# Optimization experiments

Measured on AMD Instinct MI355X. Metric: run time of the kernel, lower is better.

The kernel has to match this reference:

```python
import jax, jax.numpy as jnp
import numpy as np

B, L, D_MODEL = 1, 1024, 768
H = 12            # num_heads == num_key_value_heads
FDIM = 16         # feature_dim
HEAD_DIM = D_MODEL // H  # 64
EPS = 1e-12
R2 = np.sqrt(2.0)
RD = np.sqrt(float(FDIM))        # sqrt(16) = 4
RRD = np.sqrt(RD)                # sqrt(4) = 2


def setup_inputs() -> dict:
    key = jax.random.key(0)
    ks = jax.random.split(key, 5)
    s = 1.0 / np.sqrt(D_MODEL)
    return {
        "hidden_states": jax.random.normal(ks[0], (B, L, D_MODEL), dtype=jnp.float32),
        "Wq": jax.random.normal(ks[1], (D_MODEL, H * FDIM), dtype=jnp.float32) * s,
        "Wk": jax.random.normal(ks[2], (D_MODEL, H * FDIM), dtype=jnp.float32) * s,
        "Wv": jax.random.normal(ks[3], (D_MODEL, D_MODEL), dtype=jnp.float32) * s,
        "Wo": jax.random.normal(ks[4], (D_MODEL, D_MODEL), dtype=jnp.float32) * s,
    }


def taylor_exp_feature_map(x):
    # x: (b, h, l, FDIM) -> (b, h, l, 1 + FDIM + FDIM^2)
    x2 = (x[..., :, None] * x[..., None, :]).reshape(*x.shape[:-1], FDIM * FDIM) / R2
    ones = jnp.ones((*x.shape[:-1], 1), dtype=x.dtype)
    return jnp.concatenate([ones, x / RRD, x2 / RD], axis=-1)


def reference(hidden_states, Wq, Wk, Wv, Wo):
    b, l, _ = hidden_states.shape
    q = (hidden_states @ Wq).reshape(b, l, H, FDIM).transpose(0, 2, 1, 3)
    k = (hidden_states @ Wk).reshape(b, l, H, FDIM).transpose(0, 2, 1, 3)
    v = (hidden_states @ Wv).reshape(b, l, H, HEAD_DIM).transpose(0, 2, 1, 3)
    q = taylor_exp_feature_map(q)  # (b,h,l,Dexp)
    k = taylor_exp_feature_map(k)  # (b,h,l,Dexp)
    # causal linear attention: y_t = q_t . cumsum_t(k_s v_s^T) / (q_t . cumsum_t(k_s) + eps)
    kv = k[..., :, None] * v[..., None, :]          # (b,h,l,Dexp,hd)
    kv_cum = jnp.cumsum(kv, axis=2)                  # (b,h,l,Dexp,hd)
    num = jnp.einsum('bhln,bhlnd->bhld', q, kv_cum)  # (b,h,l,hd)
    k_cum = jnp.cumsum(k, axis=2)                    # (b,h,l,Dexp)
    den = jnp.einsum('bhln,bhln->bhl', q, k_cum)[..., None] + EPS
    y = num / den                                    # (b,h,l,hd)
    y = y.transpose(0, 2, 1, 3).reshape(b, l, H * HEAD_DIM)
    return y @ Wo
```

## Files before the change

### kernel.cpp

```cpp
#include <hip/hip_runtime.h>

#define C2 0.17677669529663687f

typedef __attribute__((ext_vector_type(8))) short short8;
typedef __attribute__((ext_vector_type(8))) unsigned short ushort8;
typedef __attribute__((ext_vector_type(4))) float f32x4;

__device__ __forceinline__ unsigned short f2bf(float x) {
    union { float f; unsigned u; } v; v.f = x;
    unsigned r = v.u + 0x7fffu + ((v.u >> 16) & 1u);
    return (unsigned short)(r >> 16);
}
__device__ __forceinline__ float bf2f(unsigned short u) {
    union { unsigned u; float f; } v; v.u = ((unsigned)u) << 16;
    return v.f;
}

__device__ __forceinline__ void gemm_inblk_splitk(
    const float* __restrict__ A, const float* __restrict__ W,
    float* __restrict__ out, int row0, int n0, int outcol0, int ldw, int outld)
{
    __shared__ unsigned short Al[2][2][64][40];
    __shared__ unsigned short Bl[2][2][64][40];
    __shared__ float red[64][65];
    const int tid = threadIdx.x;
    const int g = tid >> 8;
    const int t = tid & 255;
    const int lane = t & 63, wave4 = t >> 6;
    const int wm = wave4 & 1, wn = wave4 >> 1;
    const int quad = lane >> 4, lr = lane & 15;
    const int k0base = g * 384;

    f32x4 acc[2][2] = {{{0.f,0.f,0.f,0.f},{0.f,0.f,0.f,0.f}},
                       {{0.f,0.f,0.f,0.f},{0.f,0.f,0.f,0.f}}};

    float4 ra[2], rb[2];
    #pragma unroll
    for (int l = 0; l < 2; ++l) {
        int idx = t + l * 256;
        ra[l] = *(const float4*)&A[(size_t)(row0 + (idx >> 3)) * 768 + k0base + (idx & 7) * 4];
        rb[l] = *(const float4*)&W[(size_t)(k0base + (idx >> 4)) * ldw + n0 + (idx & 15) * 4];
    }
    #pragma unroll
    for (int l = 0; l < 2; ++l) {
        int idx = t + l * 256;
        *(ushort4*)&Al[g][0][idx >> 3][(idx & 7) * 4] =
            make_ushort4(f2bf(ra[l].x), f2bf(ra[l].y), f2bf(ra[l].z), f2bf(ra[l].w));
        int kr = idx >> 4, nq = (idx & 15) * 4;
        int col = (((kr >> 3) ^ ((idx & 15) >> 2)) << 3) | (kr & 7);
        Bl[g][0][nq + 0][col] = f2bf(rb[l].x);
        Bl[g][0][nq + 1][col] = f2bf(rb[l].y);
        Bl[g][0][nq + 2][col] = f2bf(rb[l].z);
        Bl[g][0][nq + 3][col] = f2bf(rb[l].w);
    }
    __syncthreads();

    const int ITER = 12;
    #pragma unroll
    for (int i = 0; i < ITER; ++i) {
        const int cur = i & 1, nxt = cur ^ 1;
        float4 na[2], nb[2];
        if (i + 1 < ITER) {
            int kn = k0base + (i + 1) * 32;
            #pragma unroll
            for (int l = 0; l < 2; ++l) {
                int idx = t + l * 256;
                na[l] = *(const float4*)&A[(size_t)(row0 + (idx >> 3)) * 768 + kn + (idx & 7) * 4];
                nb[l] = *(const float4*)&W[(size_t)(kn + (idx >> 4)) * ldw + n0 + (idx & 15) * 4];
            }
        }
        short8 af[2], bfr[2];
        #pragma unroll
        for (int mi = 0; mi < 2; ++mi)
            af[mi] = *(const short8*)&Al[g][cur][wm * 32 + mi * 16 + lr][quad << 3];
        #pragma unroll
        for (int ni = 0; ni < 2; ++ni) {
            int csw = quad ^ ((wn * 2 + ni) & 3);
            bfr[ni] = *(const short8*)&Bl[g][cur][wn * 32 + ni * 16 + lr][csw << 3];
        }
        #pragma unroll
        for (int mi = 0; mi < 2; ++mi)
            #pragma unroll
            for (int ni = 0; ni < 2; ++ni)
                acc[mi][ni] = __builtin_amdgcn_mfma_f32_16x16x32_bf16(af[mi], bfr[ni], acc[mi][ni], 0, 0, 0);
        if (i + 1 < ITER) {
            #pragma unroll
            for (int l = 0; l < 2; ++l) {
                int idx = t + l * 256;
                *(ushort4*)&Al[g][nxt][idx >> 3][(idx & 7) * 4] =
                    make_ushort4(f2bf(na[l].x), f2bf(na[l].y), f2bf(na[l].z), f2bf(na[l].w));
                int kr = idx >> 4, nq = (idx & 15) * 4;
                int col = (((kr >> 3) ^ ((idx & 15) >> 2)) << 3) | (kr & 7);
                Bl[g][nxt][nq + 0][col] = f2bf(nb[l].x);
                Bl[g][nxt][nq + 1][col] = f2bf(nb[l].y);
                Bl[g][nxt][nq + 2][col] = f2bf(nb[l].z);
                Bl[g][nxt][nq + 3][col] = f2bf(nb[l].w);
            }
        }
        __syncthreads();
    }
    if (g == 1) {
        #pragma unroll
        for (int mi = 0; mi < 2; ++mi)
            #pragma unroll
            for (int ni = 0; ni < 2; ++ni)
                #pragma unroll
                for (int r = 0; r < 4; ++r)
                    red[wm * 32 + mi * 16 + quad * 4 + r][wn * 32 + ni * 16 + lr] = acc[mi][ni][r];
    }
    __syncthreads();
    if (g == 0) {
        #pragma unroll
        for (int mi = 0; mi < 2; ++mi)
            #pragma unroll
            for (int ni = 0; ni < 2; ++ni)
                #pragma unroll
                for (int r = 0; r < 4; ++r) {
                    int rr = wm * 32 + mi * 16 + quad * 4 + r;
                    int cc = wn * 32 + ni * 16 + lr;
                    out[(size_t)(row0 + rr) * outld + outcol0 + cc] = acc[mi][ni][r] + red[rr][cc];
                }
    }
}

__global__ __launch_bounds__(512) void gemm_qkv_mfma(
    const float* __restrict__ H, const float* __restrict__ Wq,
    const float* __restrict__ Wk, const float* __restrict__ Wv,
    float* __restrict__ out)
{
    const int nt = blockIdx.x, mt = blockIdx.y;
    const float* W; int ldw, n0;
    if (nt < 3)      { W = Wq; ldw = 192; n0 = nt * 64; }
    else if (nt < 6) { W = Wk; ldw = 192; n0 = (nt - 3) * 64; }
    else             { W = Wv; ldw = 768; n0 = (nt - 6) * 64; }
    gemm_inblk_splitk(H, W, out, mt * 64, n0, nt * 64, ldw, 1152);
}

__global__ __launch_bounds__(512) void gemm_wo_mfma(
    const float* __restrict__ Y, const float* __restrict__ Wo, float* __restrict__ out)
{
    const int nt = blockIdx.x, mt = blockIdx.y;
    gemm_inblk_splitk(Y, Wo, out, mt * 64, nt * 64, nt * 64, 768, 768);
}

__global__ __launch_bounds__(256) void chunk_state_k(
    const float* __restrict__ qkv, unsigned short* __restrict__ St, float* __restrict__ z)
{
    const int c = blockIdx.x, h = blockIdx.y;
    __shared__ float Kc[64][17];
    __shared__ unsigned short Pk[320][72];
    __shared__ unsigned short Vt[80][72];
    const int tid = threadIdx.x;
    const int lane = tid & 63, wave = tid >> 6;
    const int quad = lane >> 4, lr = lane & 15;

    {
        int s = tid >> 2, f4 = (tid & 3) * 4;
        float4 kv = *(const float4*)&qkv[(size_t)(c * 64 + s) * 1152 + 192 + h * 16 + f4];
        Kc[s][f4 + 0] = kv.x; Kc[s][f4 + 1] = kv.y; Kc[s][f4 + 2] = kv.z; Kc[s][f4 + 3] = kv.w;
    }
    #pragma unroll
    for (int l = 0; l < 4; ++l) {
        int idx = tid + l * 256;
        int s = idx >> 4, d4 = (idx & 15) * 4;
        float4 vv = *(const float4*)&qkv[(size_t)(c * 64 + s) * 1152 + 384 + h * 64 + d4];
        Vt[d4 + 0][s] = f2bf(vv.x);
        Vt[d4 + 1][s] = f2bf(vv.y);
        Vt[d4 + 2][s] = f2bf(vv.z);
        Vt[d4 + 3][s] = f2bf(vv.w);
    }
    for (int idx = tid; idx < 16 * 72; idx += 256) {
        int rr = 64 + idx / 72, ss = idx % 72;
        Vt[rr][ss] = (rr == 64 && ss < 64) ? (unsigned short)0x3F80 : (unsigned short)0;
    }
    __syncthreads();
    for (int idx = tid; idx < 2880; idx += 256) {
        int n = idx / 9, s8 = (idx % 9) * 8;
        short8 v8;
        #pragma unroll
        for (int tt = 0; tt < 8; ++tt) {
            int s = s8 + tt;
            float ph = 0.f;
            if (s < 64 && n < 273) {
                if (n == 0) ph = 1.f;
                else if (n < 17) ph = Kc[s][n - 1] * 0.5f;
                else { int m = n - 17; ph = Kc[s][m >> 4] * Kc[s][m & 15] * C2; }
            }
            v8[tt] = (short)f2bf(ph);
        }
        *(short8*)&Pk[n][s8] = v8;
    }
    __syncthreads();

    f32x4 acc[5][5];
    #pragma unroll
    for (int a = 0; a < 5; ++a)
        #pragma unroll
        for (int b = 0; b < 5; ++b) acc[a][b] = (f32x4){0.f, 0.f, 0.f, 0.f};
    #pragma unroll
    for (int ks = 0; ks < 2; ++ks) {
        short8 af[5], bfr[5];
        #pragma unroll
        for (int mt = 0; mt < 5; ++mt)
            af[mt] = *(const short8*)&Vt[mt * 16 + lr][ks * 32 + quad * 8];
        #pragma unroll
        for (int nt = 0; nt < 5; ++nt)
            bfr[nt] = *(const short8*)&Pk[(wave * 5 + nt) * 16 + lr][ks * 32 + quad * 8];
        #pragma unroll
        for (int mt = 0; mt < 5; ++mt)
            #pragma unroll
            for (int nt = 0; nt < 5; ++nt)
                acc[mt][nt] = __builtin_amdgcn_mfma_f32_16x16x32_bf16(af[mt], bfr[nt], acc[mt][nt], 0, 0, 0);
    }
    unsigned short* Sbt = St + (size_t)(h * 16 + c) * 18432;
    float* zb = z + (h * 16 + c) * 273;
    #pragma unroll
    for (int nt = 0; nt < 5; ++nt) {
        int n = (wave * 5 + nt) * 16 + lr;
        if (n < 288) {
            #pragma unroll
            for (int mt = 0; mt < 4; ++mt)
                #pragma unroll
                for (int r = 0; r < 4; ++r)
                    Sbt[(mt * 16 + quad * 4 + r) * 288 + n] =
                        (n < 273) ? f2bf(acc[mt][nt][r]) : (unsigned short)0;
            if (quad == 0 && n < 273) zb[n] = acc[4][nt][0];
        }
    }
}

__global__ __launch_bounds__(256) void scan_state_k(unsigned short* __restrict__ St, float* __restrict__ z)
{
    const int NV = 12 * 64 * 36;
    int gid = blockIdx.x * 256 + threadIdx.x;
    if (gid < NV) {
        int hh = gid / (64 * 36), rem = gid % (64 * 36);
        int d = rem / 36, nb = rem % 36;
        unsigned short* p = St + (size_t)hh * 16 * 18432 + d * 288 + nb * 8;
        ushort8 v[16];
        #pragma unroll
        for (int cc = 0; cc < 16; ++cc) v[cc] = *(const ushort8*)(p + (size_t)cc * 18432);
        float run[8] = {0.f,0.f,0.f,0.f,0.f,0.f,0.f,0.f};
        #pragma unroll
        for (int cc = 0; cc < 16; ++cc) {
            ushort8 w;
            #pragma unroll
            for (int j = 0; j < 8; ++j) {
                w[j] = f2bf(run[j]);
                run[j] += bf2f(v[cc][j]);
            }
            *(ushort8*)(p + (size_t)cc * 18432) = w;
        }
    } else if (gid < NV + 12 * 273) {
        int e2 = gid - NV, hh = e2 / 273, n = e2 % 273;
        float* p = z + hh * 16 * 273 + n;
        float v[16];
        #pragma unroll
        for (int cc = 0; cc < 16; ++cc) v[cc] = p[cc * 273];
        float run = 0.f;
        #pragma unroll
        for (int cc = 0; cc < 16; ++cc) { p[cc * 273] = run; run += v[cc]; }
    }
}

__global__ __launch_bounds__(256) void chunk_out_k(
    const float* __restrict__ qkv, const unsigned short* __restrict__ St, const float* __restrict__ z,
    float* __restrict__ y)
{
    const int c = blockIdx.x, h = blockIdx.y;
    __shared__ float Qc[64][17];
    __shared__ unsigned short Aq[64][40];
    __shared__ unsigned short Kb[64][40];
    __shared__ unsigned short Pq[64][360];
    __shared__ unsigned short Vt[64][72];
    __shared__ float zl[288];
    __shared__ float dpart[6][64];
    const int tid = threadIdx.x;
    const int lane = tid & 63, wave = tid >> 6;
    const int wm = wave & 1, wn = wave >> 1;
    const int quad = lane >> 4, lr = lane & 15;

    const unsigned short* Sgt = St + (size_t)(h * 16 + c) * 18432;
    short8 sfr[2][9];
    #pragma unroll
    for (int ni = 0; ni < 2; ++ni)
        #pragma unroll
        for (int ks = 0; ks < 9; ++ks)
            sfr[ni][ks] = *(const short8*)&Sgt[(wn * 32 + ni * 16 + lr) * 288 + ks * 32 + quad * 8];

    {
        int s = tid >> 2, f4 = (tid & 3) * 4;
        const float* base = &qkv[(size_t)(c * 64 + s) * 1152 + h * 16];
        float4 qv = *(const float4*)&base[f4];
        float4 kv = *(const float4*)&base[192 + f4];
        Qc[s][f4 + 0] = qv.x; Qc[s][f4 + 1] = qv.y; Qc[s][f4 + 2] = qv.z; Qc[s][f4 + 3] = qv.w;
        *(ushort4*)&Aq[s][f4] = make_ushort4(f2bf(qv.x), f2bf(qv.y), f2bf(qv.z), f2bf(qv.w));
        *(ushort4*)&Kb[s][f4] = make_ushort4(f2bf(kv.x), f2bf(kv.y), f2bf(kv.z), f2bf(kv.w));
        *(ushort4*)&Aq[s][16 + (tid & 3) * 4] = make_ushort4(0, 0, 0, 0);
        *(ushort4*)&Kb[s][16 + (tid & 3) * 4] = make_ushort4(0, 0, 0, 0);
    }
    #pragma unroll
    for (int l = 0; l < 4; ++l) {
        int idx = tid + l * 256;
        int ss = idx >> 4, d4 = (idx & 15) * 4;
        float4 vv = *(const float4*)&qkv[(size_t)(c * 64 + ss) * 1152 + 384 + h * 64 + d4];
        Vt[d4 + 0][ss] = f2bf(vv.x);
        Vt[d4 + 1][ss] = f2bf(vv.y);
        Vt[d4 + 2][ss] = f2bf(vv.z);
        Vt[d4 + 3][ss] = f2bf(vv.w);
    }
    const float* zg = z + (h * 16 + c) * 273;
    for (int idx = tid; idx < 288; idx += 256) zl[idx] = (idx < 273) ? zg[idx] : 0.f;
    __syncthreads();

    f32x4 accS[2][2] = {{{0.f,0.f,0.f,0.f},{0.f,0.f,0.f,0.f}},
                        {{0.f,0.f,0.f,0.f},{0.f,0.f,0.f,0.f}}};
    {
        short8 af[2], bfr[2];
        #pragma unroll
        for (int mi = 0; mi < 2; ++mi)
            af[mi] = *(const short8*)&Aq[wm * 32 + mi * 16 + lr][quad * 8];
        #pragma unroll
        for (int ni = 0; ni < 2; ++ni)
            bfr[ni] = *(const short8*)&Kb[wn * 32 + ni * 16 + lr][quad * 8];
        #pragma unroll
        for (int mi = 0; mi < 2; ++mi)
            #pragma unroll
            for (int ni = 0; ni < 2; ++ni)
                accS[mi][ni] = __builtin_amdgcn_mfma_f32_16x16x32_bf16(af[mi], bfr[ni], accS[mi][ni], 0, 0, 0);
    }

    {
        int i = lane;
        float qr[16];
        #pragma unroll
        for (int f = 0; f < 16; ++f) qr[f] = Qc[i][f];
        float dp = 0.f;
        int n0 = wave * 72;
        for (int n = n0; n < n0 + 72; ++n) {
            float ph;
            if (n == 0) ph = 1.f;
            else if (n < 17) ph = qr[n - 1] * 0.5f;
            else if (n < 273) { int m = n - 17; ph = qr[m >> 4] * qr[m & 15] * C2; }
            else ph = 0.f;
            Pq[i][n] = f2bf(ph);
            dp += ph * zl[n];
        }
        dpart[wave][i] = dp;
    }

    #pragma unroll
    for (int mi = 0; mi < 2; ++mi) {
        float rs[4] = {0.f, 0.f, 0.f, 0.f};
        #pragma unroll
        for (int ni = 0; ni < 2; ++ni)
            #pragma unroll
            for (int r = 0; r < 4; ++r) {
                int i = wm * 32 + mi * 16 + quad * 4 + r;
                int j = wn * 32 + ni * 16 + lr;
                float u = accS[mi][ni][r];
                float sc = (j <= i) ? (1.f + 0.25f * u + u * u * (1.f / 32.f)) : 0.f;
                rs[r] += sc;
                Pq[i][288 + j] = f2bf(sc);
            }
        #pragma unroll
        for (int r = 0; r < 4; ++r) {
            float v = rs[r];
            v += __shfl_xor(v, 1);
            v += __shfl_xor(v, 2);
            v += __shfl_xor(v, 4);
            v += __shfl_xor(v, 8);
            if (lr == 0) dpart[4 + wn][wm * 32 + mi * 16 + quad * 4 + r] = v;
        }
    }
    __syncthreads();

    f32x4 acc[2][2] = {{{0.f,0.f,0.f,0.f},{0.f,0.f,0.f,0.f}},
                       {{0.f,0.f,0.f,0.f},{0.f,0.f,0.f,0.f}}};
    #pragma unroll
    for (int ks = 0; ks < 11; ++ks) {
        short8 af[2], bfr[2];
        #pragma unroll
        for (int mi = 0; mi < 2; ++mi)
            af[mi] = *(const short8*)&Pq[wm * 32 + mi * 16 + lr][ks * 32 + quad * 8];
        #pragma unroll
        for (int ni = 0; ni < 2; ++ni)
            bfr[ni] = (ks < 9)
                ? sfr[ni][ks]
                : *(const short8*)&Vt[wn * 32 + ni * 16 + lr][(ks - 9) * 32 + quad * 8];
        #pragma unroll
        for (int mi = 0; mi < 2; ++mi)
            #pragma unroll
            for (int ni = 0; ni < 2; ++ni)
                acc[mi][ni] = __builtin_amdgcn_mfma_f32_16x16x32_bf16(af[mi], bfr[ni], acc[mi][ni], 0, 0, 0);
    }

    #pragma unroll
    for (int mi = 0; mi < 2; ++mi)
        #pragma unroll
        for (int r = 0; r < 4; ++r) {
            int i = wm * 32 + mi * 16 + quad * 4 + r;
            float den = dpart[0][i] + dpart[1][i] + dpart[2][i] +
                        dpart[3][i] + dpart[4][i] + dpart[5][i] + 1e-12f;
            float rden = 1.f / den;
            #pragma unroll
            for (int ni = 0; ni < 2; ++ni)
                y[(size_t)(c * 64 + i) * 768 + h * 64 + wn * 32 + ni * 16 + lr] = acc[mi][ni][r] * rden;
        }
}

extern "C" void kernel_launch(void* const* d_in, const int* in_sizes, int n_in,
                              void* d_out, int out_size, void* d_ws, size_t ws_size,
                              hipStream_t stream) {
    const float* hs = (const float*)d_in[0];
    const float* Wq = (const float*)d_in[1];
    const float* Wk = (const float*)d_in[2];
    const float* Wv = (const float*)d_in[3];
    const float* Wo = (const float*)d_in[4];
    float* out = (float*)d_out;
    float* ws  = (float*)d_ws;

    float* qkv = ws;
    float* yb  = ws + 1179648;
    unsigned short* St = (unsigned short*)(ws + 1966080);
    float* zb  = ws + 5320704;

    gemm_qkv_mfma<<<dim3(18, 16), 512, 0, stream>>>(hs, Wq, Wk, Wv, qkv);
    chunk_state_k<<<dim3(16, 12), 256, 0, stream>>>(qkv, St, zb);
    scan_state_k <<<121, 256, 0, stream>>>(St, zb);
    chunk_out_k  <<<dim3(16, 12), 256, 0, stream>>>(qkv, St, zb, yb);
    gemm_wo_mfma <<<dim3(12, 16), 512, 0, stream>>>(yb, Wo, out);
}
```

Measured before the change: 134.9 us.

## Double waves per block in chunk state and output kernels

Both chunk kernels move from 256 to 512 threads (8 waves), and the MFMA tile work is split across more waves. chunk_state_k now assigns the 20 N-tiles round-robin across waves, and chunk_out_k gives each wave a 16-column slice with 12 denominator partials. With only 192 blocks, the intent is more in-flight waves per block to hide latency and spread MFMA and feature-map work. This costs extra reduction partials, some idle waves in the round-robin split, and fewer registers per thread.

```diff
diff --git a/kernel.cpp b/kernel.cpp
--- a/kernel.cpp
+++ b/kernel.cpp
@@ -143,8 +143,8 @@
     gemm_inblk_splitk(Y, Wo, out, mt * 64, nt * 64, nt * 64, 768, 768);
 }
 
-__global__ __launch_bounds__(256) void chunk_state_k(
-    const float* __restrict__ qkv, unsigned short* __restrict__ St, float* __restrict__ z)
+__global__ __launch_bounds__(512) void chunk_state_k(
+    const float* __restrict__ qkv, unsigned short* __restrict__ St, float* __restrict__ zb)
 {
     const int c = blockIdx.x, h = blockIdx.y;
     __shared__ float Kc[64][17];
@@ -154,14 +154,14 @@
     const int lane = tid & 63, wave = tid >> 6;
     const int quad = lane >> 4, lr = lane & 15;
 
-    {
+    if (tid < 256) {
         int s = tid >> 2, f4 = (tid & 3) * 4;
         float4 kv = *(const float4*)&qkv[(size_t)(c * 64 + s) * 1152 + 192 + h * 16 + f4];
         Kc[s][f4 + 0] = kv.x; Kc[s][f4 + 1] = kv.y; Kc[s][f4 + 2] = kv.z; Kc[s][f4 + 3] = kv.w;
     }
     #pragma unroll
-    for (int l = 0; l < 4; ++l) {
-        int idx = tid + l * 256;
+    for (int l = 0; l < 2; ++l) {
+        int idx = tid + l * 512;
         int s = idx >> 4, d4 = (idx & 15) * 4;
         float4 vv = *(const float4*)&qkv[(size_t)(c * 64 + s) * 1152 + 384 + h * 64 + d4];
         Vt[d4 + 0][s] = f2bf(vv.x);
@@ -169,12 +169,12 @@
         Vt[d4 + 2][s] = f2bf(vv.z);
         Vt[d4 + 3][s] = f2bf(vv.w);
     }
-    for (int idx = tid; idx < 16 * 72; idx += 256) {
+    for (int idx = tid; idx < 16 * 72; idx += 512) {
         int rr = 64 + idx / 72, ss = idx % 72;
         Vt[rr][ss] = (rr == 64 && ss < 64) ? (unsigned short)0x3F80 : (unsigned short)0;
     }
     __syncthreads();
-    for (int idx = tid; idx < 2880; idx += 256) {
+    for (int idx = tid; idx < 2880; idx += 512) {
         int n = idx / 9, s8 = (idx % 9) * 8;
         short8 v8;
         #pragma unroll
@@ -192,39 +192,44 @@
     }
     __syncthreads();
 
-    f32x4 acc[5][5];
-    #pragma unroll
-    for (int a = 0; a < 5; ++a)
-        #pragma unroll
-        for (int b = 0; b < 5; ++b) acc[a][b] = (f32x4){0.f, 0.f, 0.f, 0.f};
+    f32x4 acc[5][3];
+    #pragma unroll
+    for (int mt = 0; mt < 5; ++mt)
+        #pragma unroll
+        for (int nt = 0; nt < 3; ++nt) acc[mt][nt] = (f32x4){0.f, 0.f, 0.f, 0.f};
     #pragma unroll
     for (int ks = 0; ks < 2; ++ks) {
-        short8 af[5], bfr[5];
+        short8 af[5], bfr[3];
         #pragma unroll
         for (int mt = 0; mt < 5; ++mt)
             af[mt] = *(const short8*)&Vt[mt * 16 + lr][ks * 32 + quad * 8];
         #pragma unroll
-        for (int nt = 0; nt < 5; ++nt)
-            bfr[nt] = *(const short8*)&Pk[(wave * 5 + nt) * 16 + lr][ks * 32 + quad * 8];
+        for (int nt = 0; nt < 3; ++nt)
+            if (wave + 8 * nt < 20)
+                bfr[nt] = *(const short8*)&Pk[(wave + 8 * nt) * 16 + lr][ks * 32 + quad * 8];
         #pragma unroll
         for (int mt = 0; mt < 5; ++mt)
             #pragma unroll
-            for (int nt = 0; nt < 5; ++nt)
-                acc[mt][nt] = __builtin_amdgcn_mfma_f32_16x16x32_bf16(af[mt], bfr[nt], acc[mt][nt], 0, 0, 0);
+            for (int nt = 0; nt < 3; ++nt)
+                if (wave + 8 * nt < 20)
+                    acc[mt][nt] = __builtin_amdgcn_mfma_f32_16x16x32_bf16(af[mt], bfr[nt], acc[mt][nt], 0, 0, 0);
     }
     unsigned short* Sbt = St + (size_t)(h * 16 + c) * 18432;
-    float* zb = z + (h * 16 + c) * 273;
-    #pragma unroll
-    for (int nt = 0; nt < 5; ++nt) {
-        int n = (wave * 5 + nt) * 16 + lr;
-        if (n < 288) {
-            #pragma unroll
-            for (int mt = 0; mt < 4; ++mt)
+    float* zp = zb + (h * 16 + c) * 273;
+    #pragma unroll
+    for (int nt = 0; nt < 3; ++nt) {
+        int tile = wave + 8 * nt;
+        if (tile < 20) {
+            int n = tile * 16 + lr;
+            if (n < 288) {
                 #pragma unroll
-                for (int r = 0; r < 4; ++r)
-                    Sbt[(mt * 16 + quad * 4 + r) * 288 + n] =
-                        (n < 273) ? f2bf(acc[mt][nt][r]) : (unsigned short)0;
-            if (quad == 0 && n < 273) zb[n] = acc[4][nt][0];
+                for (int mt = 0; mt < 4; ++mt)
+                    #pragma unroll
+                    for (int r = 0; r < 4; ++r)
+                        Sbt[(mt * 16 + quad * 4 + r) * 288 + n] =
+                            (n < 273) ? f2bf(acc[mt][nt][r]) : (unsigned short)0;
+                if (quad == 0 && n < 273) zp[n] = acc[4][nt][0];
+            }
         }
     }
 }
@@ -263,7 +268,7 @@
     }
 }
 
-__global__ __launch_bounds__(256) void chunk_out_k(
+__global__ __launch_bounds__(512) void chunk_out_k(
     const float* __restrict__ qkv, const unsigned short* __restrict__ St, const float* __restrict__ z,
     float* __restrict__ y)
 {
@@ -274,21 +279,19 @@
     __shared__ unsigned short Pq[64][360];
     __shared__ unsigned short Vt[64][72];
     __shared__ float zl[288];
-    __shared__ float dpart[6][64];
+    __shared__ float dpart[12][64];
     const int tid = threadIdx.x;
     const int lane = tid & 63, wave = tid >> 6;
+    const int quad = lane >> 4, lr = lane & 15;
     const int wm = wave & 1, wn = wave >> 1;
-    const int quad = lane >> 4, lr = lane & 15;
 
     const unsigned short* Sgt = St + (size_t)(h * 16 + c) * 18432;
-    short8 sfr[2][9];
-    #pragma unroll
-    for (int ni = 0; ni < 2; ++ni)
-        #pragma unroll
-        for (int ks = 0; ks < 9; ++ks)
-            sfr[ni][ks] = *(const short8*)&Sgt[(wn * 32 + ni * 16 + lr) * 288 + ks * 32 + quad * 8];
-
-    {
+    short8 sfr[9];
+    #pragma unroll
+    for (int ks = 0; ks < 9; ++ks)
+        sfr[ks] = *(const short8*)&Sgt[(wn * 16 + lr) * 288 + ks * 32 + quad * 8];
+
+    if (tid < 256) {
         int s = tid >> 2, f4 = (tid & 3) * 4;
         const float* base = &qkv[(size_t)(c * 64 + s) * 1152 + h * 16];
         float4 qv = *(const float4*)&base[f4];
@@ -300,8 +303,8 @@
         *(ushort4*)&Kb[s][16 + (tid & 3) * 4] = make_ushort4(0, 0, 0, 0);
     }
     #pragma unroll
-    for (int l = 0; l < 4; ++l) {
-        int idx = tid + l * 256;
+    for (int l = 0; l < 2; ++l) {
+        int idx = tid + l * 512;
         int ss = idx >> 4, d4 = (idx & 15) * 4;
         float4 vv = *(const float4*)&qkv[(size_t)(c * 64 + ss) * 1152 + 384 + h * 64 + d4];
         Vt[d4 + 0][ss] = f2bf(vv.x);
@@ -310,24 +313,17 @@
         Vt[d4 + 3][ss] = f2bf(vv.w);
     }
     const float* zg = z + (h * 16 + c) * 273;
-    for (int idx = tid; idx < 288; idx += 256) zl[idx] = (idx < 273) ? zg[idx] : 0.f;
-    __syncthreads();
-
-    f32x4 accS[2][2] = {{{0.f,0.f,0.f,0.f},{0.f,0.f,0.f,0.f}},
-                        {{0.f,0.f,0.f,0.f},{0.f,0.f,0.f,0.f}}};
+    for (int idx = tid; idx < 288; idx += 512) zl[idx] = (idx < 273) ? zg[idx] : 0.f;
+    __syncthreads();
+
+    f32x4 accS[2] = {{0.f,0.f,0.f,0.f},{0.f,0.f,0.f,0.f}};
     {
-        short8 af[2], bfr[2];
-        #pragma unroll
-        for (int mi = 0; mi < 2; ++mi)
-            af[mi] = *(const short8*)&Aq[wm * 32 + mi * 16 + lr][quad * 8];
-        #pragma unroll
-        for (int ni = 0; ni < 2; ++ni)
-            bfr[ni] = *(const short8*)&Kb[wn * 32 + ni * 16 + lr][quad * 8];
-        #pragma unroll
-        for (int mi = 0; mi < 2; ++mi)
-            #pragma unroll
-            for (int ni = 0; ni < 2; ++ni)
-                accS[mi][ni] = __builtin_amdgcn_mfma_f32_16x16x32_bf16(af[mi], bfr[ni], accS[mi][ni], 0, 0, 0);
+        short8 bfr = *(const short8*)&Kb[wn * 16 + lr][quad * 8];
+        #pragma unroll
+        for (int mi = 0; mi < 2; ++mi) {
+            short8 af = *(const short8*)&Aq[wm * 32 + mi * 16 + lr][quad * 8];
+            accS[mi] = __builtin_amdgcn_mfma_f32_16x16x32_bf16(af, bfr, accS[mi], 0, 0, 0);
+        }
     }
 
     {
@@ -336,8 +332,8 @@
         #pragma unroll
         for (int f = 0; f < 16; ++f) qr[f] = Qc[i][f];
         float dp = 0.f;
-        int n0 = wave * 72;
-        for (int n = n0; n < n0 + 72; ++n) {
+        int n0 = wave * 36;
+        for (int n = n0; n < n0 + 36; ++n) {
             float ph;
             if (n == 0) ph = 1.f;
             else if (n < 17) ph = qr[n - 1] * 0.5f;
@@ -351,18 +347,16 @@
 
     #pragma unroll
     for (int mi = 0; mi < 2; ++mi) {
-        float rs[4] = {0.f, 0.f, 0.f, 0.f};
-        #pragma unroll
-        for (int ni = 0; ni < 2; ++ni)
-            #pragma unroll
-            for (int r = 0; r < 4; ++r) {
-                int i = wm * 32 + mi * 16 + quad * 4 + r;
-                int j = wn * 32 + ni * 16 + lr;
-                float u = accS[mi][ni][r];
-                float sc = (j <= i) ? (1.f + 0.25f * u + u * u * (1.f / 32.f)) : 0.f;
-                rs[r] += sc;
-                Pq[i][288 + j] = f2bf(sc);
-            }
+        float rs[4];
+        #pragma unroll
+        for (int r = 0; r < 4; ++r) {
+            int i = wm * 32 + mi * 16 + quad * 4 + r;
+            int j = wn * 16 + lr;
+            float u = accS[mi][r];
+            float sc = (j <= i) ? (1.f + 0.25f * u + u * u * (1.f / 32.f)) : 0.f;
+            rs[r] = sc;
+            Pq[i][288 + j] = f2bf(sc);
+        }
         #pragma unroll
         for (int r = 0; r < 4; ++r) {
             float v = rs[r];
@@ -370,29 +364,22 @@
             v += __shfl_xor(v, 2);
             v += __shfl_xor(v, 4);
             v += __shfl_xor(v, 8);
-            if (lr == 0) dpart[4 + wn][wm * 32 + mi * 16 + quad * 4 + r] = v;
-        }
-    }
-    __syncthreads();
-
-    f32x4 acc[2][2] = {{{0.f,0.f,0.f,0.f},{0.f,0.f,0.f,0.f}},
-                       {{0.f,0.f,0.f,0.f},{0.f,0.f,0.f,0.f}}};
+            if (lr == 0) dpart[8 + wn][wm * 32 + mi * 16 + quad * 4 + r] = v;
+        }
+    }
+    __syncthreads();
+
+    f32x4 acc[2] = {{0.f,0.f,0.f,0.f},{0.f,0.f,0.f,0.f}};
     #pragma unroll
     for (int ks = 0; ks < 11; ++ks) {
-        short8 af[2], bfr[2];
-        #pragma unroll
-        for (int mi = 0; mi < 2; ++mi)
-            af[mi] = *(const short8*)&Pq[wm * 32 + mi * 16 + lr][ks * 32 + quad * 8];
-        #pragma unroll
-        for (int ni = 0; ni < 2; ++ni)
-            bfr[ni] = (ks < 9)
-                ? sfr[ni][ks]
-                : *(const short8*)&Vt[wn * 32 + ni * 16 + lr][(ks - 9) * 32 + quad * 8];
-        #pragma unroll
-        for (int mi = 0; mi < 2; ++mi)
-            #pragma unroll
-            for (int ni = 0; ni < 2; ++ni)
-                acc[mi][ni] = __builtin_amdgcn_mfma_f32_16x16x32_bf16(af[mi], bfr[ni], acc[mi][ni], 0, 0, 0);
+        short8 bfr = (ks < 9)
+            ? sfr[ks]
+            : *(const short8*)&Vt[wn * 16 + lr][(ks - 9) * 32 + quad * 8];
+        #pragma unroll
+        for (int mi = 0; mi < 2; ++mi) {
+            short8 af = *(const short8*)&Pq[wm * 32 + mi * 16 + lr][ks * 32 + quad * 8];
+            acc[mi] = __builtin_amdgcn_mfma_f32_16x16x32_bf16(af, bfr, acc[mi], 0, 0, 0);
+        }
     }
 
     #pragma unroll
@@ -400,12 +387,11 @@
         #pragma unroll
         for (int r = 0; r < 4; ++r) {
             int i = wm * 32 + mi * 16 + quad * 4 + r;
-            float den = dpart[0][i] + dpart[1][i] + dpart[2][i] +
-                        dpart[3][i] + dpart[4][i] + dpart[5][i] + 1e-12f;
+            float den = 1e-12f;
+            #pragma unroll
+            for (int w = 0; w < 12; ++w) den += dpart[w][i];
             float rden = 1.f / den;
-            #pragma unroll
-            for (int ni = 0; ni < 2; ++ni)
-                y[(size_t)(c * 64 + i) * 768 + h * 64 + wn * 32 + ni * 16 + lr] = acc[mi][ni][r] * rden;
+            y[(size_t)(c * 64 + i) * 768 + h * 64 + wn * 16 + lr] = acc[mi][r] * rden;
         }
 }
 
@@ -426,8 +412,8 @@
     float* zb  = ws + 5320704;
 
     gemm_qkv_mfma<<<dim3(18, 16), 512, 0, stream>>>(hs, Wq, Wk, Wv, qkv);
-    chunk_state_k<<<dim3(16, 12), 256, 0, stream>>>(qkv, St, zb);
+    chunk_state_k<<<dim3(16, 12), 512, 0, stream>>>(qkv, St, zb);
     scan_state_k <<<121, 256, 0, stream>>>(St, zb);
-    chunk_out_k  <<<dim3(16, 12), 256, 0, stream>>>(qkv, St, zb, yb);
+    chunk_out_k  <<<dim3(16, 12), 512, 0, stream>>>(qkv, St, zb, yb);
     gemm_wo_mfma <<<dim3(12, 16), 512, 0, stream>>>(yb, Wo, out);
 }
```

Measured after the change: 120.5 us. -10.7%, faster.
